# Kernel tuning notes

Hardware: AMD Instinct MI355X
Metric: run time of the kernel (lower is better)

Reference implementation:

```python
import jax, jax.numpy as jnp
import numpy as np

C = 512
GROUPS = 32
EPS = 1e-6


def setup_inputs() -> dict:
    key = jax.random.key(0)
    ks = jax.random.split(key, 10)
    B, H, W = 4, 64, 64
    s = 1.0 / np.sqrt(C)
    return {
        "x": jax.random.normal(ks[0], (B, C, H, W), dtype=jnp.float32),
        "gn_weight": jnp.ones((C,), jnp.float32),
        "gn_bias": jnp.zeros((C,), jnp.float32),
        "Wq": jax.random.normal(ks[1], (C, C), jnp.float32) * s,
        "bq": jnp.zeros((C,), jnp.float32),
        "Wk": jax.random.normal(ks[2], (C, C), jnp.float32) * s,
        "bk": jnp.zeros((C,), jnp.float32),
        "Wv": jax.random.normal(ks[3], (C, C), jnp.float32) * s,
        "bv": jnp.zeros((C,), jnp.float32),
        "Wo": jax.random.normal(ks[4], (C, C), jnp.float32) * s,
        "bo": jnp.zeros((C,), jnp.float32),
    }


def _group_norm(x, weight, bias):
    B, Ch, H, W = x.shape
    xg = x.reshape(B, GROUPS, Ch // GROUPS, H, W)
    mean = jnp.mean(xg, axis=(2, 3, 4), keepdims=True)
    var = jnp.var(xg, axis=(2, 3, 4), keepdims=True)
    xg = (xg - mean) * jax.lax.rsqrt(var + EPS)
    h = xg.reshape(B, Ch, H, W)
    return h * weight[None, :, None, None] + bias[None, :, None, None]


def reference(x, gn_weight, gn_bias, Wq, bq, Wk, bk, Wv, bv, Wo, bo):
    B, Ch, H, W = x.shape
    h = _group_norm(x, gn_weight, gn_bias)
    # [B, N, C] with N = H*W spatial tokens
    h = h.reshape(B, Ch, H * W).transpose(0, 2, 1)
    q = h @ Wq.T + bq
    k = h @ Wk.T + bk
    v = h @ Wv.T + bv
    scale = 1.0 / jnp.sqrt(jnp.asarray(Ch, x.dtype))
    scores = jnp.einsum("bnc,bmc->bnm", q, k) * scale  # [B, N, N]
    attn = jax.nn.softmax(scores, axis=-1)
    out = jnp.einsum("bnm,bmc->bnc", attn, v)
    out = out @ Wo.T + bo  # Dropout(0.0) is identity
    out = out.transpose(0, 2, 1).reshape(B, Ch, H, W)
    return x + out
```

## Files before the change

kernel.cpp:

```cpp
#include <hip/hip_runtime.h>
#include <hip/hip_bf16.h>

typedef __attribute__((ext_vector_type(8))) short bf16x8;
typedef __attribute__((ext_vector_type(4))) short bf16x4;
typedef __attribute__((ext_vector_type(4))) float f32x4;

__device__ __forceinline__ short f2bf(float f){
  __hip_bfloat16 h = __float2bfloat16(f);
  return __builtin_bit_cast(short, h);
}
__device__ __forceinline__ float bf2f(short s){
  unsigned u = ((unsigned)(unsigned short)s) << 16;
  return __builtin_bit_cast(float, u);
}

__device__ __forceinline__ void gload_lds16(const short* g, char* l){
  __builtin_amdgcn_global_load_lds(
      (const __attribute__((address_space(1))) void*)g,
      (__attribute__((address_space(3))) void*)l, 16, 0, 0);
}

#define SB0() __builtin_amdgcn_sched_barrier(0)
#define BARRIER() do{ SB0(); __builtin_amdgcn_s_barrier(); }while(0)

__global__ __launch_bounds__(256) void gn_stats(const float* __restrict__ x,
                                                float* __restrict__ stats){
  int b = blockIdx.x >> 5, g = blockIdx.x & 31;
  const float4* p = (const float4*)(x + ((long long)b*512 + g*16)*4096);
  float s = 0.f, s2 = 0.f;
  for (int i = threadIdx.x; i < 16384; i += 256){
    float4 v = p[i];
    s  += v.x + v.y + v.z + v.w;
    s2 += v.x*v.x + v.y*v.y + v.z*v.z + v.w*v.w;
  }
  #pragma unroll
  for (int o = 32; o; o >>= 1){ s += __shfl_xor(s, o); s2 += __shfl_xor(s2, o); }
  __shared__ float rs[4], rs2[4];
  int wid = threadIdx.x >> 6;
  if ((threadIdx.x & 63) == 0){ rs[wid] = s; rs2[wid] = s2; }
  __syncthreads();
  if (threadIdx.x == 0){
    float S  = rs[0]+rs[1]+rs[2]+rs[3];
    float S2 = rs2[0]+rs2[1]+rs2[2]+rs2[3];
    float mean = S * (1.f/65536.f);
    float var  = S2 * (1.f/65536.f) - mean*mean;
    stats[blockIdx.x*2]   = mean;
    stats[blockIdx.x*2+1] = rsqrtf(var + 1e-6f);
  }
}

__global__ __launch_bounds__(256) void gn_apply(const float* __restrict__ x,
                                                const float* __restrict__ stats,
                                                const float* __restrict__ gw,
                                                const float* __restrict__ gb,
                                                short* __restrict__ h){
  __shared__ float tile[128][65];
  int b  = blockIdx.y;
  int n0 = blockIdx.x * 64;
  int t  = threadIdx.x;
  const float* xb = x + (long long)b*512*4096;
  for (int cc = 0; cc < 4; cc++){
    int c0 = cc*128;
    #pragma unroll
    for (int r = 0; r < 128; r += 4){
      int c = r + (t >> 6);
      tile[c][t & 63] = xb[(long long)(c0+c)*4096 + n0 + (t & 63)];
    }
    __syncthreads();
    int n = t >> 2, cp = (t & 3)*32;
    short tmp[32];
    #pragma unroll
    for (int j = 0; j < 32; j++){
      int c = c0 + cp + j;
      float mean = stats[(b*32 + (c >> 4))*2];
      float rstd = stats[(b*32 + (c >> 4))*2 + 1];
      float v = (tile[cp+j][n] - mean)*rstd*gw[c] + gb[c];
      tmp[j] = f2bf(v);
    }
    long long ho = ((long long)b*4096 + n0 + n)*512 + c0 + cp;
    #pragma unroll
    for (int j2 = 0; j2 < 4; j2++){
      bf16x8 v8;
      #pragma unroll
      for (int e = 0; e < 8; e++) v8[e] = tmp[j2*8 + e];
      *(bf16x8*)&h[ho + j2*8] = v8;
    }
    __syncthreads();
  }
}

__global__ __launch_bounds__(256) void f2bf_all(
    const float* __restrict__ w0, const float* __restrict__ w1,
    const float* __restrict__ w2, const float* __restrict__ w3,
    short* __restrict__ o0, short* __restrict__ o1,
    short* __restrict__ o2, short* __restrict__ o3){
  int idx = blockIdx.x*256 + threadIdx.x;
  int m = idx >> 15, r = idx & 32767;
  const float* src = (m==0) ? w0 : (m==1) ? w1 : (m==2) ? w2 : w3;
  short* dst       = (m==0) ? o0 : (m==1) ? o1 : (m==2) ? o2 : o3;
  const float4* p = (const float4*)src + (long long)r*2;
  float4 a = p[0], c = p[1];
  bf16x8 v;
  v[0]=f2bf(a.x); v[1]=f2bf(a.y); v[2]=f2bf(a.z); v[3]=f2bf(a.w);
  v[4]=f2bf(c.x); v[5]=f2bf(c.y); v[6]=f2bf(c.z); v[7]=f2bf(c.w);
  *(bf16x8*)&dst[(long long)r*8] = v;
}

__global__ __launch_bounds__(256) void reduce_den(const float* __restrict__ partial,
                                                  float* __restrict__ inv_den,
                                                  int nrows){
  int r = blockIdx.x*256 + threadIdx.x;
  if (r >= nrows) return;
  const float4* p = (const float4*)(partial + (long long)r*16);
  float4 a = p[0], b = p[1], c = p[2], d = p[3];
  float s = a.x+a.y+a.z+a.w + b.x+b.y+b.z+b.w + c.x+c.y+c.z+c.w + d.x+d.y+d.z+d.w;
  inv_den[r] = 1.f / s;
}

template<int MODE, int BN, int SWZ>
__global__ __launch_bounds__(512, 2) void gemmF(
    const short* __restrict__ A, const short* __restrict__ Bw,
    const float* __restrict__ bias,
    void* __restrict__ outp, const float* __restrict__ resid,
    int M, int Nn, int Kd,
    long long sA, long long sB, long long sO, float scale,
    const float* __restrict__ dptr, float* __restrict__ partial)
{
  constexpr int WARPS_N = BN/64;
  constexpr int WARPS_M = 8/WARPS_N;
  constexpr int WM = 256/WARPS_M;
  constexpr int MF = WM/16;
  constexpr int QR = MF/4;
  constexpr int ABYT = 32768;
  constexpr int BBYT = BN*128;
  constexpr int BUFSZ = ABYT + BBYT;
  constexpr int BH = BBYT/16384;
  extern __shared__ char smem[];

  int bx, by, bz;
  if constexpr (SWZ == 1){
    int id = blockIdx.x;
    int xcd = id & 7, s = id >> 3;
    int region = xcd + ((s >> 4) << 3);
    int o = s & 15;
    bz = region >> 4;
    bx = (region & 3)*4 + (o & 3);
    by = ((region >> 2) & 3)*4 + (o >> 2);
  } else if constexpr (SWZ == 2){
    int id = blockIdx.x;
    int xcd = id & 7, s = id >> 3;
    int combo = xcd*2 + (s & 1);
    by = combo & 3; bz = combo >> 2;
    bx = s >> 1;
  } else { bx = blockIdx.x; by = blockIdx.y; bz = blockIdx.z; }

  const short* Ab = A + bz*sA;
  const short* Bb = Bw + bz*sB;
  const int m0 = bx*256, n0 = by*BN;
  const int t = threadIdx.x;
  const int lane = t & 63, wid = t >> 6;
  const int g = lane >> 4, lr = lane & 15;
  const int wr = wid / WARPS_N, wc = wid % WARPS_N;
  const long long KdLL = Kd;

  const int r0 = t >> 3, c8 = t & 7;

  auto STAGE_A = [&](int kt, int buf, int h){
    char* d = smem + buf*BUFSZ + h*16384 + t*16;
    #pragma unroll
    for (int j = 0; j < 2; j++){
      int row = h*128 + j*64 + r0;
      gload_lds16(Ab + (long long)(m0+row)*KdLL + (long long)kt*64 + ((c8 ^ (row&7))*8),
                  d + j*8192);
    }
  };
  auto STAGE_B = [&](int kt, int buf, int h){
    char* d = smem + buf*BUFSZ + ABYT + h*16384 + t*16;
    #pragma unroll
    for (int j = 0; j < 2; j++){
      int row = h*128 + j*64 + r0;
      gload_lds16(Bb + (long long)(n0+row)*KdLL + (long long)kt*64 + ((c8 ^ (row&7))*8),
                  d + j*8192);
    }
  };

  int roA[MF], swA[MF], roB[4], swB[4];
  #pragma unroll
  for (int mf = 0; mf < MF; mf++){
    int ra = wr*WM + mf*16 + lr;
    roA[mf] = (ra>>7)*16384 + (ra&127)*128; swA[mf] = ra & 7;
  }
  #pragma unroll
  for (int nf = 0; nf < 4; nf++){
    int rb = wc*64 + nf*16 + lr;
    roB[nf] = ABYT + (rb>>7)*16384 + (rb&127)*128; swB[nf] = rb & 7;
  }

  f32x4 acc[MF][4];
  #pragma unroll
  for (int i = 0; i < MF; i++)
    #pragma unroll
    for (int j = 0; j < 4; j++)
      acc[i][j] = f32x4{0.f,0.f,0.f,0.f};
  bf16x8 av[2][QR][2], bv[4][2];

  #define RD_AV(SET, Q, BASE) do{                                         \
    _Pragma("unroll")                                                     \
    for (int _i = 0; _i < QR; _i++)                                       \
      _Pragma("unroll")                                                   \
      for (int _ks = 0; _ks < 2; _ks++){                                  \
        int _x = (Q)*QR + _i;                                             \
        av[SET][_i][_ks] = *(const bf16x8*)((BASE) + roA[_x] +            \
                            (((_ks*4+g) ^ swA[_x])<<4));                  \
      } }while(0)

  #define RD_BV(BASE) do{                                                 \
    _Pragma("unroll")                                                     \
    for (int _n = 0; _n < 4; _n++)                                        \
      _Pragma("unroll")                                                   \
      for (int _ks = 0; _ks < 2; _ks++)                                   \
        bv[_n][_ks] = *(const bf16x8*)((BASE) + roB[_n] +                 \
                            (((_ks*4+g) ^ swB[_n])<<4));                  \
    }while(0)

  #define MFMA_PH(Q, SET) do{                                             \
    __builtin_amdgcn_s_setprio(1);                                        \
    _Pragma("unroll")                                                     \
    for (int _ks = 0; _ks < 2; _ks++)                                     \
      _Pragma("unroll")                                                   \
      for (int _n = 0; _n < 4; _n++)                                      \
        _Pragma("unroll")                                                 \
        for (int _i = 0; _i < QR; _i++){                                  \
          if constexpr (MODE == 1 || MODE == 2)                           \
            acc[(Q)*QR+_i][_n] = __builtin_amdgcn_mfma_f32_16x16x32_bf16( \
              av[SET][_i][_ks], bv[_n][_ks], acc[(Q)*QR+_i][_n], 0,0,0);  \
          else                                                            \
            acc[(Q)*QR+_i][_n] = __builtin_amdgcn_mfma_f32_16x16x32_bf16( \
              bv[_n][_ks], av[SET][_i][_ks], acc[(Q)*QR+_i][_n], 0,0,0);  \
        }                                                                 \
    __builtin_amdgcn_s_setprio(0); }while(0)

  #define WAIT_LGKM_JI() do{                                              \
    if constexpr (QR == 2) asm volatile("s_waitcnt lgkmcnt(4)":::"memory");\
    else                   asm volatile("s_waitcnt lgkmcnt(2)":::"memory");\
    SB0(); }while(0)

  const int NT = Kd >> 6;

  STAGE_A(0,0,0); STAGE_A(0,0,1);
  STAGE_B(0,0,0); if constexpr (BH==2) STAGE_B(0,0,1);
  STAGE_B(1,1,0); if constexpr (BH==2) STAGE_B(1,1,1);
  if constexpr (BH==2) asm volatile("s_waitcnt vmcnt(4)":::"memory");
  else                 asm volatile("s_waitcnt vmcnt(2)":::"memory");
  SB0();
  __builtin_amdgcn_s_barrier();
  RD_AV(0, 0, smem);

  for (int kt = 0; kt < NT; ++kt){
    char* bc  = smem + (kt & 1)*BUFSZ;
    char* bn_ = smem + ((kt & 1)^1)*BUFSZ;
    RD_BV(bc);
    RD_AV(1, 1, bc);
    if (kt+1 < NT) STAGE_A(kt+1, (kt&1)^1, 0);
    BARRIER();
    WAIT_LGKM_JI();
    MFMA_PH(0, 0);
    BARRIER();
    RD_AV(0, 2, bc);
    if (kt+1 < NT) STAGE_A(kt+1, (kt&1)^1, 1);
    BARRIER();
    WAIT_LGKM_JI();
    MFMA_PH(1, 1);
    BARRIER();
    RD_AV(1, 3, bc);
    if (kt+2 < NT) STAGE_B(kt+2, kt&1, 0);
    BARRIER();
    if (kt+2 < NT) asm volatile("s_waitcnt vmcnt(2)":::"memory");
    else           asm volatile("s_waitcnt vmcnt(0)":::"memory");
    SB0();
    WAIT_LGKM_JI();
    MFMA_PH(2, 0);
    BARRIER();
    if (kt+1 < NT) RD_AV(0, 0, bn_);
    if constexpr (BH==2){ if (kt+2 < NT) STAGE_B(kt+2, kt&1, 1); }
    BARRIER();
    if (kt+1 < NT){ WAIT_LGKM_JI(); }
    else { asm volatile("s_waitcnt lgkmcnt(0)":::"memory"); SB0(); }
    MFMA_PH(3, 1);
    BARRIER();
  }

  if constexpr (MODE == 0){
    short* outb = (short*)outp + bz*sO;
    const bool hb = (bias != nullptr);
    #pragma unroll
    for (int mi = 0; mi < MF; mi++){
      int row = m0 + wr*WM + mi*16 + lr;
      #pragma unroll
      for (int ni = 0; ni < 4; ni++){
        int col = n0 + wc*64 + ni*16 + g*4;
        float b0=0.f,b1=0.f,b2=0.f,b3=0.f;
        if (hb){ float4 bb = *(const float4*)&bias[col]; b0=bb.x; b1=bb.y; b2=bb.z; b3=bb.w; }
        bf16x4 pk;
        pk[0] = f2bf((acc[mi][ni][0] + b0)*scale);
        pk[1] = f2bf((acc[mi][ni][1] + b1)*scale);
        pk[2] = f2bf((acc[mi][ni][2] + b2)*scale);
        pk[3] = f2bf((acc[mi][ni][3] + b3)*scale);
        *(bf16x4*)&outb[(long long)row*Nn + col] = pk;
      }
    }
  } else if constexpr (MODE == 4){
    short* outb = (short*)outp + bz*sO;
    float* rowpart = (float*)smem;
    constexpr float LOG2E = 1.4426950408889634f;
    #pragma unroll
    for (int mi = 0; mi < MF; mi++){
      int lrow = wr*WM + mi*16 + lr;
      int row  = m0 + lrow;
      float rs = 0.f;
      #pragma unroll
      for (int ni = 0; ni < 4; ni++){
        int col = n0 + wc*64 + ni*16 + g*4;
        bf16x4 pk;
        #pragma unroll
        for (int i = 0; i < 4; i++){
          float p = exp2f(acc[mi][ni][i]*LOG2E);
          rs += p;
          pk[i] = f2bf(p);
        }
        *(bf16x4*)&outb[(long long)row*Nn + col] = pk;
      }
      rs += __shfl_xor(rs, 16);
      rs += __shfl_xor(rs, 32);
      if (g == 0) rowpart[lrow*WARPS_N + wc] = rs;
    }
    __syncthreads();
    if (t < 256){
      float s2 = 0.f;
      #pragma unroll
      for (int j = 0; j < WARPS_N; j++) s2 += rowpart[t*WARPS_N + j];
      partial[((long long)bz*4096 + m0 + t)*16 + by] = s2;
    }
  } else if constexpr (MODE == 5){
    short* outb = (short*)outp + bz*sO;
    const float* dd = dptr + (long long)bz*M;
    #pragma unroll
    for (int mi = 0; mi < MF; mi++){
      int row = m0 + wr*WM + mi*16 + lr;
      float inv = dd[row];
      #pragma unroll
      for (int ni = 0; ni < 4; ni++){
        int col = n0 + wc*64 + ni*16 + g*4;
        bf16x4 pk;
        #pragma unroll
        for (int i = 0; i < 4; i++) pk[i] = f2bf(acc[mi][ni][i]*inv);
        *(bf16x4*)&outb[(long long)row*Nn + col] = pk;
      }
    }
  } else if constexpr (MODE == 1){
    short* outb = (short*)outp + bz*sO;
    #pragma unroll
    for (int ni = 0; ni < 4; ni++){
      int col = n0 + wc*64 + ni*16 + lr;
      float bv2 = bias ? bias[col] : 0.f;
      #pragma unroll
      for (int mi = 0; mi < MF; mi++){
        int row = m0 + wr*WM + mi*16 + g*4;
        bf16x4 pk;
        #pragma unroll
        for (int i = 0; i < 4; i++) pk[i] = f2bf((acc[mi][ni][i] + bv2)*scale);
        *(bf16x4*)&outb[(long long)col*M + row] = pk;
      }
    }
  } else {
    float* outb = (float*)outp + bz*sO;
    const float* rx = resid + bz*sO;
    #pragma unroll
    for (int ni = 0; ni < 4; ni++){
      int col = n0 + wc*64 + ni*16 + lr;
      float bv2 = bias[col];
      #pragma unroll
      for (int mi = 0; mi < MF; mi++){
        int row = m0 + wr*WM + mi*16 + g*4;
        long long off = (long long)col*M + row;
        float4 xr = *(const float4*)&rx[off];
        float4 o;
        o.x = acc[mi][ni][0] + bv2 + xr.x;
        o.y = acc[mi][ni][1] + bv2 + xr.y;
        o.z = acc[mi][ni][2] + bv2 + xr.z;
        o.w = acc[mi][ni][3] + bv2 + xr.w;
        *(float4*)&outb[off] = o;
      }
    }
  }
  #undef RD_AV
  #undef RD_BV
  #undef MFMA_PH
  #undef WAIT_LGKM_JI
}

extern "C" void kernel_launch(void* const* d_in, const int* in_sizes, int n_in,
                              void* d_out, int out_size, void* d_ws, size_t ws_size,
                              hipStream_t stream)
{
  const float* x   = (const float*)d_in[0];
  const float* gnw = (const float*)d_in[1];
  const float* gnb = (const float*)d_in[2];
  const float* Wq  = (const float*)d_in[3];
  const float* bq  = (const float*)d_in[4];
  const float* Wk  = (const float*)d_in[5];
  const float* bk  = (const float*)d_in[6];
  const float* Wv  = (const float*)d_in[7];
  const float* bvp = (const float*)d_in[8];
  const float* Wo  = (const float*)d_in[9];
  const float* bo  = (const float*)d_in[10];
  float* out = (float*)d_out;

  char* ws = (char*)d_ws;
  const size_t MB = 1ull << 20;
  short* h      = (short*)(ws);
  short* q      = (short*)(ws + 16*MB);
  short* kmat   = (short*)(ws + 32*MB);
  short* vt     = (short*)(ws + 48*MB);
  short* ao     = (short*)(ws + 64*MB);
  short* wqb    = (short*)(ws + 80*MB);
  short* wkb    = wqb + 262144;
  short* wvb    = wkb + 262144;
  short* wob    = wvb + 262144;
  float* stats  = (float*)(ws + 82*MB);
  float* inv_den= (float*)(ws + 82*MB + 8192);
  float* partial= (float*)(ws + 83*MB);
  short* S      = (short*)(ws + 84*MB);

  const int LDS256 = 131072, LDS128 = 98304;
  hipFuncSetAttribute(reinterpret_cast<const void*>(&gemmF<4,256,1>),
                      hipFuncAttributeMaxDynamicSharedMemorySize, LDS256);
  hipFuncSetAttribute(reinterpret_cast<const void*>(&gemmF<4,256,0>),
                      hipFuncAttributeMaxDynamicSharedMemorySize, LDS256);
  hipFuncSetAttribute(reinterpret_cast<const void*>(&gemmF<0,128,0>),
                      hipFuncAttributeMaxDynamicSharedMemorySize, LDS128);
  hipFuncSetAttribute(reinterpret_cast<const void*>(&gemmF<1,128,0>),
                      hipFuncAttributeMaxDynamicSharedMemorySize, LDS128);
  hipFuncSetAttribute(reinterpret_cast<const void*>(&gemmF<2,128,0>),
                      hipFuncAttributeMaxDynamicSharedMemorySize, LDS128);
  hipFuncSetAttribute(reinterpret_cast<const void*>(&gemmF<5,128,2>),
                      hipFuncAttributeMaxDynamicSharedMemorySize, LDS128);
  hipFuncSetAttribute(reinterpret_cast<const void*>(&gemmF<5,128,0>),
                      hipFuncAttributeMaxDynamicSharedMemorySize, LDS128);

  dim3 blk(256);
  dim3 blk512(512);
  gn_stats<<<dim3(128), blk, 0, stream>>>(x, stats);
  gn_apply<<<dim3(64,4), blk, 0, stream>>>(x, stats, gnw, gnb, h);
  f2bf_all<<<dim3(512), blk, 0, stream>>>(Wq, Wk, Wv, Wo, wqb, wkb, wvb, wob);

  const long long sTok = 4096ll*512;
  const long long sS   = 4096ll*4096;
  const float qscale = 0.044194173824159216f;

  gemmF<0,128,0><<<dim3(16,4,4), blk512, LDS128, stream>>>(h, wqb, bq,  q,    nullptr, 4096, 512, 512, sTok, 0, sTok, qscale, nullptr, nullptr);
  gemmF<0,128,0><<<dim3(16,4,4), blk512, LDS128, stream>>>(h, wkb, bk,  kmat, nullptr, 4096, 512, 512, sTok, 0, sTok, 1.f, nullptr, nullptr);
  gemmF<1,128,0><<<dim3(16,4,4), blk512, LDS128, stream>>>(h, wvb, bvp, vt,   nullptr, 4096, 512, 512, sTok, 0, sTok, 1.f, nullptr, nullptr);

  if (ws_size >= 212*MB){
    gemmF<4,256,1><<<dim3(1024), blk512, LDS256, stream>>>(q, kmat, nullptr, S, nullptr, 4096, 4096, 512, sTok, sTok, sS, 1.f, nullptr, partial);
    reduce_den<<<dim3(64), blk, 0, stream>>>(partial, inv_den, 16384);
    gemmF<5,128,2><<<dim3(256), blk512, LDS128, stream>>>(S, vt, nullptr, ao, nullptr, 4096, 512, 4096, sS, sTok, sTok, 1.f, inv_den, nullptr);
  } else {
    for (int b = 0; b < 4; b++){
      gemmF<4,256,0><<<dim3(16,16,1), blk512, LDS256, stream>>>(q + b*sTok, kmat + b*sTok, nullptr, S, nullptr, 4096, 4096, 512, 0, 0, 0, 1.f, nullptr, partial);
      reduce_den<<<dim3(16), blk, 0, stream>>>(partial, inv_den, 4096);
      gemmF<5,128,0><<<dim3(16,4,1), blk512, LDS128, stream>>>(S, vt + b*sTok, nullptr, ao + b*sTok, nullptr, 4096, 512, 4096, 0, 0, 0, 1.f, inv_den, nullptr);
    }
  }

  gemmF<2,128,0><<<dim3(16,4,4), blk512, LDS128, stream>>>(ao, wob, bo, out, x, 4096, 512, 512, sTok, 0, sTok, 1.f, nullptr, nullptr);
}
```

Baseline: 318.1 us.

## Replace phased 4-quarter GEMM pipeline with simple double-buffered per-tile loop

```diff
diff --git a/kernel.cpp b/kernel.cpp
--- a/kernel.cpp
+++ b/kernel.cpp
@@ -21,7 +21,6 @@
 }
 
 #define SB0() __builtin_amdgcn_sched_barrier(0)
-#define BARRIER() do{ SB0(); __builtin_amdgcn_s_barrier(); }while(0)
 
 __global__ __launch_bounds__(256) void gn_stats(const float* __restrict__ x,
                                                 float* __restrict__ stats){
@@ -130,11 +129,11 @@
   constexpr int WARPS_M = 8/WARPS_N;
   constexpr int WM = 256/WARPS_M;
   constexpr int MF = WM/16;
-  constexpr int QR = MF/4;
   constexpr int ABYT = 32768;
   constexpr int BBYT = BN*128;
   constexpr int BUFSZ = ABYT + BBYT;
   constexpr int BH = BBYT/16384;
+  constexpr int LOADS = 4 + 2*BH;
   extern __shared__ char smem[];
 
   int bx, by, bz;
@@ -202,92 +201,54 @@
     #pragma unroll
     for (int j = 0; j < 4; j++)
       acc[i][j] = f32x4{0.f,0.f,0.f,0.f};
-  bf16x8 av[2][QR][2], bv[4][2];
-
-  #define RD_AV(SET, Q, BASE) do{                                         \
-    _Pragma("unroll")                                                     \
-    for (int _i = 0; _i < QR; _i++)                                       \
-      _Pragma("unroll")                                                   \
-      for (int _ks = 0; _ks < 2; _ks++){                                  \
-        int _x = (Q)*QR + _i;                                             \
-        av[SET][_i][_ks] = *(const bf16x8*)((BASE) + roA[_x] +            \
-                            (((_ks*4+g) ^ swA[_x])<<4));                  \
-      } }while(0)
-
-  #define RD_BV(BASE) do{                                                 \
-    _Pragma("unroll")                                                     \
-    for (int _n = 0; _n < 4; _n++)                                        \
-      _Pragma("unroll")                                                   \
-      for (int _ks = 0; _ks < 2; _ks++)                                   \
-        bv[_n][_ks] = *(const bf16x8*)((BASE) + roB[_n] +                 \
-                            (((_ks*4+g) ^ swB[_n])<<4));                  \
-    }while(0)
-
-  #define MFMA_PH(Q, SET) do{                                             \
-    __builtin_amdgcn_s_setprio(1);                                        \
-    _Pragma("unroll")                                                     \
-    for (int _ks = 0; _ks < 2; _ks++)                                     \
-      _Pragma("unroll")                                                   \
-      for (int _n = 0; _n < 4; _n++)                                      \
-        _Pragma("unroll")                                                 \
-        for (int _i = 0; _i < QR; _i++){                                  \
-          if constexpr (MODE == 1 || MODE == 2)                           \
-            acc[(Q)*QR+_i][_n] = __builtin_amdgcn_mfma_f32_16x16x32_bf16( \
-              av[SET][_i][_ks], bv[_n][_ks], acc[(Q)*QR+_i][_n], 0,0,0);  \
-          else                                                            \
-            acc[(Q)*QR+_i][_n] = __builtin_amdgcn_mfma_f32_16x16x32_bf16( \
-              bv[_n][_ks], av[SET][_i][_ks], acc[(Q)*QR+_i][_n], 0,0,0);  \
-        }                                                                 \
-    __builtin_amdgcn_s_setprio(0); }while(0)
-
-  #define WAIT_LGKM_JI() do{                                              \
-    if constexpr (QR == 2) asm volatile("s_waitcnt lgkmcnt(4)":::"memory");\
-    else                   asm volatile("s_waitcnt lgkmcnt(2)":::"memory");\
-    SB0(); }while(0)
 
   const int NT = Kd >> 6;
 
   STAGE_A(0,0,0); STAGE_A(0,0,1);
   STAGE_B(0,0,0); if constexpr (BH==2) STAGE_B(0,0,1);
+  STAGE_A(1,1,0); STAGE_A(1,1,1);
   STAGE_B(1,1,0); if constexpr (BH==2) STAGE_B(1,1,1);
-  if constexpr (BH==2) asm volatile("s_waitcnt vmcnt(4)":::"memory");
-  else                 asm volatile("s_waitcnt vmcnt(2)":::"memory");
+  if constexpr (BH==2) asm volatile("s_waitcnt vmcnt(8)":::"memory");
+  else                 asm volatile("s_waitcnt vmcnt(6)":::"memory");
   SB0();
   __builtin_amdgcn_s_barrier();
-  RD_AV(0, 0, smem);
 
   for (int kt = 0; kt < NT; ++kt){
-    char* bc  = smem + (kt & 1)*BUFSZ;
-    char* bn_ = smem + ((kt & 1)^1)*BUFSZ;
-    RD_BV(bc);
-    RD_AV(1, 1, bc);
-    if (kt+1 < NT) STAGE_A(kt+1, (kt&1)^1, 0);
-    BARRIER();
-    WAIT_LGKM_JI();
-    MFMA_PH(0, 0);
-    BARRIER();
-    RD_AV(0, 2, bc);
-    if (kt+1 < NT) STAGE_A(kt+1, (kt&1)^1, 1);
-    BARRIER();
-    WAIT_LGKM_JI();
-    MFMA_PH(1, 1);
-    BARRIER();
-    RD_AV(1, 3, bc);
-    if (kt+2 < NT) STAGE_B(kt+2, kt&1, 0);
-    BARRIER();
-    if (kt+2 < NT) asm volatile("s_waitcnt vmcnt(2)":::"memory");
-    else           asm volatile("s_waitcnt vmcnt(0)":::"memory");
+    char* base = smem + (kt & 1)*BUFSZ;
+    bf16x8 av[MF][2], bv[4][2];
+    #pragma unroll
+    for (int n = 0; n < 4; n++)
+      #pragma unroll
+      for (int ks = 0; ks < 2; ks++)
+        bv[n][ks] = *(const bf16x8*)(base + roB[n] + (((ks*4+g) ^ swB[n])<<4));
+    #pragma unroll
+    for (int m = 0; m < MF; m++)
+      #pragma unroll
+      for (int ks = 0; ks < 2; ks++)
+        av[m][ks] = *(const bf16x8*)(base + roA[m] + (((ks*4+g) ^ swA[m])<<4));
+    #pragma unroll
+    for (int ks = 0; ks < 2; ks++)
+      #pragma unroll
+      for (int m = 0; m < MF; m++)
+        #pragma unroll
+        for (int n = 0; n < 4; n++){
+          if constexpr (MODE == 1 || MODE == 2)
+            acc[m][n] = __builtin_amdgcn_mfma_f32_16x16x32_bf16(av[m][ks], bv[n][ks], acc[m][n], 0,0,0);
+          else
+            acc[m][n] = __builtin_amdgcn_mfma_f32_16x16x32_bf16(bv[n][ks], av[m][ks], acc[m][n], 0,0,0);
+        }
     SB0();
-    WAIT_LGKM_JI();
-    MFMA_PH(2, 0);
-    BARRIER();
-    if (kt+1 < NT) RD_AV(0, 0, bn_);
-    if constexpr (BH==2){ if (kt+2 < NT) STAGE_B(kt+2, kt&1, 1); }
-    BARRIER();
-    if (kt+1 < NT){ WAIT_LGKM_JI(); }
-    else { asm volatile("s_waitcnt lgkmcnt(0)":::"memory"); SB0(); }
-    MFMA_PH(3, 1);
-    BARRIER();
+    __builtin_amdgcn_s_barrier();
+    SB0();
+    if (kt + 2 < NT){
+      STAGE_A(kt+2, kt&1, 0); STAGE_A(kt+2, kt&1, 1);
+      STAGE_B(kt+2, kt&1, 0); if constexpr (BH==2) STAGE_B(kt+2, kt&1, 1);
+      if constexpr (BH==2) asm volatile("s_waitcnt vmcnt(8)":::"memory");
+      else                 asm volatile("s_waitcnt vmcnt(6)":::"memory");
+    } else {
+      asm volatile("s_waitcnt vmcnt(0)":::"memory");
+    }
+    __builtin_amdgcn_s_barrier();
   }
 
   if constexpr (MODE == 0){
@@ -393,10 +354,6 @@
       }
     }
   }
-  #undef RD_AV
-  #undef RD_BV
-  #undef MFMA_PH
-  #undef WAIT_LGKM_JI
 }
 
 extern "C" void kernel_launch(void* const* d_in, const int* in_sizes, int n_in,
```

Measured after the change: 317.0 us. No clear change (-0.3%).
